# Optimization experiments

Hardware: AMD Instinct MI355X
Metric: run time of the kernel (lower is better)

## Reference

```python
import jax, jax.numpy as jnp
import numpy as np

L, B, N, C, H = 6, 4, 512, 512, 8
D = C // H          # head_dim = 64
MLP = 4 * C         # mlp_ratio = 4.0
EPS = 1e-6


def setup_inputs() -> dict:
    key = jax.random.key(0)
    ks = jax.random.split(key, 12)
    p = lambda k, sh: jax.random.normal(k, sh, dtype=jnp.float32) * 0.02
    return {
        "x": jax.random.normal(ks[0], (B, N, C), dtype=jnp.float32),
        "time_emb": jax.random.normal(ks[1], (B, C), dtype=jnp.float32),
        "pair_emb": jax.random.normal(ks[2], (B, H, N, N), dtype=jnp.float32) * 0.1,
        "is_padded_mask": jnp.zeros((B, 1, 1, N), dtype=bool),
        # per-block stacked params (leading dim = L blocks)
        "wq": p(ks[3], (L, C, C)),
        "wk": p(ks[4], (L, C, C)),
        "wv": p(ks[5], (L, C, C)),
        "wo": p(ks[6], (L, C, C)),
        "bo": jnp.zeros((L, C), dtype=jnp.float32),
        "w1": p(ks[7], (L, C, MLP)),
        "b1": jnp.zeros((L, MLP), dtype=jnp.float32),
        "w2": p(ks[8], (L, MLP, C)),
        "b2": jnp.zeros((L, C), dtype=jnp.float32),
        "wada": p(ks[9], (L, C, 6 * C)),
        "bada": jnp.zeros((L, 6 * C), dtype=jnp.float32),
    }


def _ln(x):
    # LayerNorm without affine, eps=1e-6 (torch elementwise_affine=False)
    mu = jnp.mean(x, axis=-1, keepdims=True)
    var = jnp.mean(jnp.square(x - mu), axis=-1, keepdims=True)
    return (x - mu) * jax.lax.rsqrt(var + EPS)


def _modulate(x, shift, scale):
    return x * (1.0 + scale[:, None, :]) + shift[:, None, :]


def reference(x, time_emb, pair_emb, is_padded_mask,
              wq, wk, wv, wo, bo, w1, b1, w2, b2, wada, bada):
    scale = D ** -0.5
    t_act = jax.nn.silu(time_emb)  # shared SiLU input to adaLN of each block
    for i in range(L):
        ada = t_act @ wada[i] + bada[i]  # (B, 6C)
        sh_msa, sc_msa, g_msa, sh_mlp, sc_mlp, g_mlp = jnp.split(ada, 6, axis=1)
        # fill_attn_mask: masked_fill padded key positions with -inf
        pair = jnp.where(is_padded_mask, -jnp.inf, pair_emb)  # (B,H,N,N)
        mx = _modulate(_ln(x), sh_msa, sc_msa)  # (B,N,C)
        q = (mx @ wq[i]).reshape(B, N, H, D)
        k = (mx @ wk[i]).reshape(B, N, H, D)
        v = (mx @ wv[i]).reshape(B, N, H, D)
        qk = jnp.einsum('bnhd,bshd->bhns', q, k) * scale  # (B,H,N,N)
        attn = jax.nn.softmax(qk + pair, axis=-1)
        o = jnp.einsum('bhns,bshd->bnhd', attn, v).reshape(B, N, C)
        o = o @ wo[i] + bo[i]
        x = x + g_msa[:, None, :] * o
        pair_emb = pair + qk  # residual on pair embedding
        h = _modulate(_ln(x), sh_mlp, sc_mlp)
        h = jax.nn.gelu(h @ w1[i] + b1[i], approximate=True) @ w2[i] + b2[i]
        x = x + g_mlp[:, None, :] * h
    return x, pair_emb
```

## Files before the change

### kernel.cpp

```cpp
#include <hip/hip_runtime.h>
#include <hip/hip_bf16.h>

#define LNUM 6
#define BB 4
#define NSEQ 512
#define CDIM 512
#define HNUM 8
#define DHEAD 64
#define MLPD 2048
#define MROWS (BB*NSEQ)

typedef __hip_bfloat16 bf16;
typedef __attribute__((ext_vector_type(4))) float f32x4;
typedef __attribute__((ext_vector_type(8))) short bf16x8;

__device__ __forceinline__ void gld_lds16(const bf16* g, bf16* l) {
  __builtin_amdgcn_global_load_lds((const __attribute__((address_space(1))) void*)g,
                                   (__attribute__((address_space(3))) void*)l, 16, 0, 0);
}

__device__ __forceinline__ float gelu_tanh(float t) {
  float u = 0.7978845608028654f * (t + 0.044715f * t * t * t);
  u = fminf(fmaxf(u, -15.f), 15.f);
  float e = __expf(2.f * u);
  return 0.5f * t * (1.f + (e - 1.f) / (e + 1.f));
}

enum { EP_BF16 = 0, EP_RESID = 2, EP_GELU = 3, EP_QKV = 4 };

template<int BM, int BN, int MODE>
__global__ __launch_bounds__(256) void gemm_nt(
    const bf16* __restrict__ A, int lda,
    const bf16* __restrict__ Bt, int ldb,
    int K, int zdiv,
    long sA1, long sA2, long sB1, long sB2, long sO1, long sO2,
    bf16* __restrict__ obf, int ldo,
    const float* __restrict__ bias,
    const float* __restrict__ ada, int gate_off,
    float* __restrict__ xres,
    bf16* __restrict__ vtout)
{
  constexpr int FM = BM / 32, FN = BN / 32;
  __shared__ bf16 lA[2 * BM * 64];
  __shared__ bf16 lB[2 * BN * 64];
  const int tid = threadIdx.x;
  const int wid = tid >> 6, lane = tid & 63;
  const int z = blockIdx.z;
  const long z1 = z / zdiv, z2 = z % zdiv;
  A  += z1 * sA1 + z2 * sA2;
  Bt += z1 * sB1 + z2 * sB2;
  const long obase = z1 * sO1 + z2 * sO2;
  const int m0 = blockIdx.x * BM;
  const int n0 = blockIdx.y * BN;
  const int wm = wid >> 1, wn = wid & 1;
  const int srow = tid >> 3, scl = tid & 7;

  f32x4 zero = {0.f, 0.f, 0.f, 0.f};
  f32x4 acc[FM][FN];
#pragma unroll
  for (int i = 0; i < FM; i++)
#pragma unroll
    for (int j = 0; j < FN; j++) acc[i][j] = zero;

  auto stage = [&](int buf, int kt) {
#pragma unroll
    for (int p = 0; p < BM / 32; p++) {
      const int rr = (p << 5) + srow;
      const int gk = (scl ^ (rr & 7)) << 3;
      gld_lds16(A + (size_t)(m0 + rr) * lda + (kt << 6) + gk,
                lA + buf * (BM * 64) + (p << 11) + (wid << 9));
    }
#pragma unroll
    for (int p = 0; p < BN / 32; p++) {
      const int rr = (p << 5) + srow;
      const int gk = (scl ^ (rr & 7)) << 3;
      gld_lds16(Bt + (size_t)(n0 + rr) * ldb + (kt << 6) + gk,
                lB + buf * (BN * 64) + (p << 11) + (wid << 9));
    }
  };

  const int rlo = lane & 15, kq = lane >> 4;
  auto compute = [&](int buf) {
#pragma unroll
    for (int kk = 0; kk < 2; kk++) {
      bf16x8 af[FM], bg[FN];
#pragma unroll
      for (int i = 0; i < FM; i++) {
        const int ra = wm * (BM / 2) + (i << 4) + rlo;
        af[i] = *(const bf16x8*)(lA + buf * (BM * 64) + (ra << 6) +
                                 ((((kk << 2) + kq) ^ (ra & 7)) << 3));
      }
#pragma unroll
      for (int j = 0; j < FN; j++) {
        const int rb2 = wn * (BN / 2) + (j << 4) + rlo;
        bg[j] = *(const bf16x8*)(lB + buf * (BN * 64) + (rb2 << 6) +
                                 ((((kk << 2) + kq) ^ (rb2 & 7)) << 3));
      }
#pragma unroll
      for (int i = 0; i < FM; i++)
#pragma unroll
        for (int j = 0; j < FN; j++)
          acc[i][j] = __builtin_amdgcn_mfma_f32_16x16x32_bf16(af[i], bg[j], acc[i][j], 0, 0, 0);
    }
  };

  const int NT = K >> 6;
  stage(0, 0);
  for (int t = 0; t < NT - 1; t++) {
    stage((t + 1) & 1, t + 1);
    constexpr int NL = (BM + BN) / 32;
    if constexpr (NL == 3)      asm volatile("s_waitcnt vmcnt(3)" ::: "memory");
    else if constexpr (NL == 4) asm volatile("s_waitcnt vmcnt(4)" ::: "memory");
    else if constexpr (NL == 6) asm volatile("s_waitcnt vmcnt(6)" ::: "memory");
    else                        asm volatile("s_waitcnt vmcnt(8)" ::: "memory");
    __builtin_amdgcn_s_barrier();
    asm volatile("" ::: "memory");
    compute(t & 1);
    asm volatile("" ::: "memory");
    __builtin_amdgcn_s_barrier();
  }
  asm volatile("s_waitcnt vmcnt(0)" ::: "memory");
  __builtin_amdgcn_s_barrier();
  asm volatile("" ::: "memory");
  compute((NT - 1) & 1);

  const int cl = lane & 15, rb = (lane >> 4) << 2;

  if (MODE == EP_QKV && n0 >= 2 * CDIM) {
    asm volatile("" ::: "memory");
    __builtin_amdgcn_s_barrier();
    bf16* lT = lA;
#pragma unroll
    for (int i = 0; i < FM; i++)
#pragma unroll
      for (int j = 0; j < FN; j++)
#pragma unroll
        for (int r = 0; r < 4; r++) {
          const int ln = wm * (BM / 2) + (i << 4) + rb + r;
          const int ld = wn * (BN / 2) + (j << 4) + cl;
          lT[ld * 72 + ln] = __float2bfloat16(acc[i][j][r]);
        }
    asm volatile("" ::: "memory");
    __builtin_amdgcn_s_barrier();
    const int b = m0 >> 9, nn = m0 & 511, h = (n0 - 2 * CDIM) >> 6;
    bf16* dst = vtout + ((size_t)(b * 8 + h) * 64) * 512;
    const int d = tid >> 2, nc = (tid & 3) << 4;
    bf16x8 v0 = *(const bf16x8*)(lT + d * 72 + nc);
    bf16x8 v1 = *(const bf16x8*)(lT + d * 72 + nc + 8);
    *(bf16x8*)(dst + (size_t)d * 512 + nn + nc) = v0;
    *(bf16x8*)(dst + (size_t)d * 512 + nn + nc + 8) = v1;
    return;
  }

#pragma unroll
  for (int i = 0; i < FM; i++) {
#pragma unroll
    for (int j = 0; j < FN; j++) {
      const int gc = n0 + wn * (BN / 2) + (j << 4) + cl;
#pragma unroll
      for (int r = 0; r < 4; r++) {
        const int gr = m0 + wm * (BM / 2) + (i << 4) + rb + r;
        float v = acc[i][j][r];
        if (MODE == EP_BF16 || MODE == EP_QKV) {
          obf[obase + (size_t)gr * ldo + gc] = __float2bfloat16(v);
        } else if (MODE == EP_RESID) {
          const int b = gr >> 9;
          float t2 = v + bias[gc];
          xres[(size_t)gr * CDIM + gc] += ada[b * (6 * CDIM) + gate_off + gc] * t2;
        } else {
          float t2 = v + bias[gc];
          obf[obase + (size_t)gr * ldo + gc] = __float2bfloat16(gelu_tanh(t2));
        }
      }
    }
  }
}

__global__ __launch_bounds__(256) void attn_fused(
    const bf16* __restrict__ qkv, const bf16* __restrict__ vt,
    const float* __restrict__ pair_in, float* __restrict__ pair_out,
    const unsigned char* __restrict__ mask,
    bf16* __restrict__ obuf, float scale)
{
  __shared__ bf16 lQ[64 * 64];
  __shared__ bf16 lK[2][64 * 64];
  __shared__ bf16 lV[2][64 * 64];
  __shared__ bf16 lP[64 * 64];
  const int tid = threadIdx.x, wid = tid >> 6, lane = tid & 63;
  const int z = blockIdx.z, b = z >> 3, h = z & 7;
  const int m0 = blockIdx.x * 64;
  const int srow = tid >> 3, scl = tid & 7;
  const bf16* Aq = qkv + (size_t)b * NSEQ * 1536 + h * 64;
  const bf16* Bk = Aq + CDIM;
  const bf16* Bv = vt + (size_t)z * DHEAD * NSEQ;
  const size_t pz = (size_t)z * NSEQ * NSEQ;
  const int rlo = lane & 15, kq = lane >> 4, cl = rlo;

#pragma unroll
  for (int r = 0; r < 2; r++) {
    const int rr = (r << 5) + srow;
    const int gk = (scl ^ (rr & 7)) << 3;
    gld_lds16(Aq + (size_t)(m0 + rr) * 1536 + gk, lQ + (r << 11) + (wid << 9));
    gld_lds16(Bk + (size_t)rr * 1536 + gk, lK[0] + (r << 11) + (wid << 9));
    gld_lds16(Bv + (size_t)rr * NSEQ + gk, lV[0] + (r << 11) + (wid << 9));
  }

  float m_run[4], l_run[4];
  f32x4 oacc[4];
  f32x4 zero = {0.f, 0.f, 0.f, 0.f};
#pragma unroll
  for (int r = 0; r < 4; r++) { m_run[r] = -INFINITY; l_run[r] = 0.f; }
#pragma unroll
  for (int j = 0; j < 4; j++) oacc[j] = zero;
  bf16x8 afq[2];

  for (int ct = 0; ct < 8; ct++) {
    const int cur = ct & 1;
    asm volatile("s_waitcnt vmcnt(0)" ::: "memory");
    __builtin_amdgcn_s_barrier();
    asm volatile("" ::: "memory");

    if (ct == 0) {
#pragma unroll
      for (int kk = 0; kk < 2; kk++) {
        const int ra = (wid << 4) + rlo;
        afq[kk] = *(const bf16x8*)(lQ + (ra << 6) + ((((kk << 2) + kq) ^ (ra & 7)) << 3));
      }
    }

    if (ct < 7) {
#pragma unroll
      for (int r = 0; r < 2; r++) {
        const int rr = (r << 5) + srow;
        const int gk = (scl ^ (rr & 7)) << 3;
        gld_lds16(Bk + (size_t)((ct + 1) * 64 + rr) * 1536 + gk,
                  lK[cur ^ 1] + (r << 11) + (wid << 9));
        gld_lds16(Bv + (size_t)rr * NSEQ + (ct + 1) * 64 + gk,
                  lV[cur ^ 1] + (r << 11) + (wid << 9));
      }
    }

    float pr[4][4];
#pragma unroll
    for (int j = 0; j < 4; j++)
#pragma unroll
      for (int r = 0; r < 4; r++)
        pr[j][r] = pair_in[pz + (size_t)(m0 + (wid << 4) + (kq << 2) + r) * NSEQ +
                           (ct * 64 + (j << 4) + cl)];
    bool mk[4];
#pragma unroll
    for (int j = 0; j < 4; j++)
      mk[j] = mask[b * NSEQ + ct * 64 + (j << 4) + cl] != 0;

    f32x4 s[4];
#pragma unroll
    for (int j = 0; j < 4; j++) s[j] = zero;
#pragma unroll
    for (int kk = 0; kk < 2; kk++)
#pragma unroll
      for (int j = 0; j < 4; j++) {
        const int rk = (j << 4) + rlo;
        bf16x8 bk = *(const bf16x8*)(lK[cur] + (rk << 6) + ((((kk << 2) + kq) ^ (rk & 7)) << 3));
        s[j] = __builtin_amdgcn_mfma_f32_16x16x32_bf16(afq[kk], bk, s[j], 0, 0, 0);
      }

    float p[4][4];
#pragma unroll
    for (int r = 0; r < 4; r++) {
      const size_t prow = pz + (size_t)(m0 + (wid << 4) + (kq << 2) + r) * NSEQ + ct * 64;
      float sf[4];
#pragma unroll
      for (int j = 0; j < 4; j++) {
        float pp = mk[j] ? -INFINITY : pr[j][r];
        sf[j] = s[j][r] * scale + pp;
        pair_out[prow + (j << 4) + cl] = sf[j];
      }
      float tm = fmaxf(fmaxf(sf[0], sf[1]), fmaxf(sf[2], sf[3]));
#pragma unroll
      for (int o = 1; o < 16; o <<= 1) tm = fmaxf(tm, __shfl_xor(tm, o));
      const float mnew = fmaxf(m_run[r], tm);
      const float fr = __expf(m_run[r] - mnew);
      float rs = 0.f;
#pragma unroll
      for (int j = 0; j < 4; j++) { p[j][r] = __expf(sf[j] - mnew); rs += p[j][r]; }
#pragma unroll
      for (int o = 1; o < 16; o <<= 1) rs += __shfl_xor(rs, o);
      l_run[r] = l_run[r] * fr + rs;
      m_run[r] = mnew;
#pragma unroll
      for (int j = 0; j < 4; j++) oacc[j][r] *= fr;
    }

#pragma unroll
    for (int j = 0; j < 4; j++)
#pragma unroll
      for (int r = 0; r < 4; r++) {
        const int row = (wid << 4) + (kq << 2) + r;
        const int col = (j << 4) + cl;
        lP[(row << 6) + (((col >> 3) ^ (row & 7)) << 3) + (col & 7)] = __float2bfloat16(p[j][r]);
      }
    asm volatile("s_waitcnt lgkmcnt(0)" ::: "memory");
    __builtin_amdgcn_sched_barrier(0);

#pragma unroll
    for (int kk = 0; kk < 2; kk++) {
      const int ra = (wid << 4) + rlo;
      bf16x8 ap = *(const bf16x8*)(lP + (ra << 6) + ((((kk << 2) + kq) ^ (ra & 7)) << 3));
#pragma unroll
      for (int j = 0; j < 4; j++) {
        const int rd = (j << 4) + rlo;
        bf16x8 bv = *(const bf16x8*)(lV[cur] + (rd << 6) + ((((kk << 2) + kq) ^ (rd & 7)) << 3));
        oacc[j] = __builtin_amdgcn_mfma_f32_16x16x32_bf16(ap, bv, oacc[j], 0, 0, 0);
      }
    }
  }

#pragma unroll
  for (int j = 0; j < 4; j++)
#pragma unroll
    for (int r = 0; r < 4; r++) {
      const int gr = m0 + (wid << 4) + (kq << 2) + r;
      const int gc = h * 64 + (j << 4) + cl;
      obuf[((size_t)b * NSEQ + gr) * CDIM + gc] = __float2bfloat16(oacc[j][r] / l_run[r]);
    }
}

__global__ __launch_bounds__(256) void ln_mod(const float* __restrict__ x,
                                              const float* __restrict__ ada,
                                              int sh_off, int sc_off,
                                              bf16* __restrict__ out)
{
  const int row = blockIdx.x;
  const int b = row >> 9;
  const float* xr = x + (size_t)row * CDIM;
  const int t = threadIdx.x;
  float2 v = ((const float2*)xr)[t];
  float s = v.x + v.y;
  float ss = v.x * v.x + v.y * v.y;
#pragma unroll
  for (int o = 32; o > 0; o >>= 1) { s += __shfl_down(s, o); ss += __shfl_down(ss, o); }
  __shared__ float red[8];
  __shared__ float mv[2];
  const int w = t >> 6, ln = t & 63;
  if (ln == 0) { red[w] = s; red[4 + w] = ss; }
  __syncthreads();
  if (t == 0) {
    float S = red[0] + red[1] + red[2] + red[3];
    float SS = red[4] + red[5] + red[6] + red[7];
    float mu = S * (1.0f / CDIM);
    float var = SS * (1.0f / CDIM) - mu * mu;
    mv[0] = mu; mv[1] = rsqrtf(var + 1e-6f);
  }
  __syncthreads();
  const float mu = mv[0], rs = mv[1];
  const float* adab = ada + b * (6 * CDIM);
  const int c = t * 2;
  float o0 = (v.x - mu) * rs * (1.0f + adab[sc_off + c])     + adab[sh_off + c];
  float o1 = (v.y - mu) * rs * (1.0f + adab[sc_off + c + 1]) + adab[sh_off + c + 1];
  out[(size_t)row * CDIM + c]     = __float2bfloat16(o0);
  out[(size_t)row * CDIM + c + 1] = __float2bfloat16(o1);
}

__global__ __launch_bounds__(256) void ada_part(const float* __restrict__ te,
                                                const float* __restrict__ wada,
                                                float* __restrict__ partial)
{
  __shared__ float ta[4][64];
  const int layer = blockIdx.z, kc = blockIdx.y;
  const int t = threadIdx.x;
  {
    const int b = t >> 6, kk = t & 63;
    float xx = te[b * CDIM + kc * 64 + kk];
    ta[b][kk] = xx / (1.f + __expf(-xx));
  }
  __syncthreads();
  const int col = blockIdx.x * 512 + t * 2;
  const float* W = wada + ((size_t)layer * CDIM + kc * 64) * 3072 + col;
  float2 acc0 = {0, 0}, acc1 = {0, 0}, acc2 = {0, 0}, acc3 = {0, 0};
#pragma unroll 8
  for (int kk = 0; kk < 64; kk++) {
    float2 w = *(const float2*)(W + (size_t)kk * 3072);
    acc0.x = fmaf(ta[0][kk], w.x, acc0.x); acc0.y = fmaf(ta[0][kk], w.y, acc0.y);
    acc1.x = fmaf(ta[1][kk], w.x, acc1.x); acc1.y = fmaf(ta[1][kk], w.y, acc1.y);
    acc2.x = fmaf(ta[2][kk], w.x, acc2.x); acc2.y = fmaf(ta[2][kk], w.y, acc2.y);
    acc3.x = fmaf(ta[3][kk], w.x, acc3.x); acc3.y = fmaf(ta[3][kk], w.y, acc3.y);
  }
  float* pp = partial + (((size_t)(layer * 8 + kc) * 4) * 3072);
  *(float2*)(pp + 0 * 3072 + col) = acc0;
  *(float2*)(pp + 1 * 3072 + col) = acc1;
  *(float2*)(pp + 2 * 3072 + col) = acc2;
  *(float2*)(pp + 3 * 3072 + col) = acc3;
}

__global__ __launch_bounds__(256) void ada_reduce(const float* __restrict__ partial,
                                                  const float* __restrict__ bada,
                                                  float* __restrict__ adab)
{
  const int idx = blockIdx.x * 256 + threadIdx.x;
  const int layer = idx / 12288, rem = idx % 12288;
  const int b = rem / 3072, col = rem % 3072;
  float acc = bada[layer * 3072 + col];
#pragma unroll
  for (int kc = 0; kc < 8; kc++)
    acc += partial[((size_t)(layer * 8 + kc) * 4 + b) * 3072 + col];
  adab[((size_t)layer * 4 + b) * 3072 + col] = acc;
}

__global__ __launch_bounds__(256) void conv_t(const float* __restrict__ src, bf16* __restrict__ dst,
                                              int R, int Ccols, long sS, long sD)
{
  src += (size_t)blockIdx.z * sS;
  dst += (size_t)blockIdx.z * sD;
  __shared__ float tb[32][33];
  const int c0 = blockIdx.x * 32, r0 = blockIdx.y * 32;
  const int tx = threadIdx.x & 31, ty = threadIdx.x >> 5;
#pragma unroll
  for (int i = ty; i < 32; i += 8) tb[i][tx] = src[(size_t)(r0 + i) * Ccols + c0 + tx];
  __syncthreads();
#pragma unroll
  for (int i = ty; i < 32; i += 8) dst[(size_t)(c0 + i) * R + r0 + tx] = __float2bfloat16(tb[tx][i]);
}

extern "C" void kernel_launch(void* const* d_in, const int* in_sizes, int n_in,
                              void* d_out, int out_size, void* d_ws, size_t ws_size,
                              hipStream_t stream)
{
  (void)in_sizes; (void)n_in; (void)out_size; (void)ws_size;
  const float* in_x    = (const float*)d_in[0];
  const float* in_te   = (const float*)d_in[1];
  const float* in_pair = (const float*)d_in[2];
  const unsigned char* in_mask = (const unsigned char*)d_in[3];
  const float* wq   = (const float*)d_in[4];
  const float* wk   = (const float*)d_in[5];
  const float* wv   = (const float*)d_in[6];
  const float* wo   = (const float*)d_in[7];
  const float* bo   = (const float*)d_in[8];
  const float* w1   = (const float*)d_in[9];
  const float* b1   = (const float*)d_in[10];
  const float* w2   = (const float*)d_in[11];
  const float* b2   = (const float*)d_in[12];
  const float* wada = (const float*)d_in[13];
  const float* bada = (const float*)d_in[14];

  float* xout = (float*)d_out;
  float* pairout = xout + (size_t)BB * NSEQ * CDIM;

  char* ws = (char*)d_ws;
  size_t off = 0;
  auto alloc = [&](size_t bytes) -> void* {
    void* p = ws + off; off += (bytes + 255) & ~(size_t)255; return p;
  };
  bf16*  wqkvT = (bf16*)alloc((size_t)LNUM * 1536 * 512 * 2);
  bf16*  woT   = (bf16*)alloc((size_t)LNUM * 512 * 512 * 2);
  bf16*  w1T   = (bf16*)alloc((size_t)LNUM * 2048 * 512 * 2);
  bf16*  w2T   = (bf16*)alloc((size_t)LNUM * 512 * 2048 * 2);
  float* adab  = (float*)alloc((size_t)LNUM * BB * 6 * CDIM * 4);
  float* apart = (float*)alloc((size_t)LNUM * 8 * BB * 3072 * 4);
  bf16*  mx    = (bf16*)alloc((size_t)MROWS * CDIM * 2);
  bf16*  qkv   = (bf16*)alloc((size_t)MROWS * 1536 * 2);
  bf16*  vt    = (bf16*)alloc((size_t)BB * HNUM * DHEAD * NSEQ * 2);
  bf16*  obuf  = (bf16*)alloc((size_t)MROWS * CDIM * 2);
  bf16*  hbuf  = (bf16*)alloc((size_t)MROWS * MLPD * 2);

  hipMemcpyAsync(xout, in_x, (size_t)MROWS * CDIM * 4, hipMemcpyDeviceToDevice, stream);

  conv_t<<<dim3(16, 16, LNUM), 256, 0, stream>>>(wq, wqkvT,               512, 512,  (long)512 * 512,  (long)1536 * 512);
  conv_t<<<dim3(16, 16, LNUM), 256, 0, stream>>>(wk, wqkvT + 512 * 512,   512, 512,  (long)512 * 512,  (long)1536 * 512);
  conv_t<<<dim3(16, 16, LNUM), 256, 0, stream>>>(wv, wqkvT + 2 * 512 * 512, 512, 512, (long)512 * 512, (long)1536 * 512);
  conv_t<<<dim3(16, 16, LNUM), 256, 0, stream>>>(wo, woT,                 512, 512,  (long)512 * 512,  (long)512 * 512);
  conv_t<<<dim3(64, 16, LNUM), 256, 0, stream>>>(w1, w1T,                 512, 2048, (long)512 * 2048, (long)2048 * 512);
  conv_t<<<dim3(16, 64, LNUM), 256, 0, stream>>>(w2, w2T,                 2048, 512, (long)2048 * 512, (long)512 * 2048);

  ada_part<<<dim3(6, 8, LNUM), 256, 0, stream>>>(in_te, wada, apart);
  ada_reduce<<<dim3(LNUM * BB * 3072 / 256), 256, 0, stream>>>(apart, bada, adab);

  const float scale = 0.125f;
  for (int i = 0; i < LNUM; i++) {
    const float* adal = adab + (size_t)i * BB * 6 * CDIM;
    ln_mod<<<MROWS, 256, 0, stream>>>(xout, adal, 0, CDIM, mx);
    gemm_nt<64, 64, EP_QKV><<<dim3(32, 24, 1), 256, 0, stream>>>(
        mx, CDIM, wqkvT + (size_t)i * 1536 * 512, CDIM, CDIM, 1,
        0, 0, 0, 0, 0, 0,
        qkv, 1536, nullptr, nullptr, 0, nullptr, vt);
    const float* pin = (i == 0) ? in_pair : pairout;
    attn_fused<<<dim3(8, 1, 32), 256, 0, stream>>>(qkv, vt, pin, pairout, in_mask, obuf, scale);
    gemm_nt<32, 64, EP_RESID><<<dim3(64, 8, 1), 256, 0, stream>>>(
        obuf, CDIM, woT + (size_t)i * CDIM * CDIM, CDIM, CDIM, 1,
        0, 0, 0, 0, 0, 0,
        nullptr, CDIM, bo + (size_t)i * CDIM, adal, 2 * CDIM, xout, nullptr);
    ln_mod<<<MROWS, 256, 0, stream>>>(xout, adal, 3 * CDIM, 4 * CDIM, mx);
    gemm_nt<64, 64, EP_GELU><<<dim3(32, 32, 1), 256, 0, stream>>>(
        mx, CDIM, w1T + (size_t)i * MLPD * CDIM, CDIM, CDIM, 1,
        0, 0, 0, 0, 0, 0,
        hbuf, MLPD, b1 + (size_t)i * MLPD, nullptr, 0, nullptr, nullptr);
    gemm_nt<32, 64, EP_RESID><<<dim3(64, 8, 1), 256, 0, stream>>>(
        hbuf, MLPD, w2T + (size_t)i * CDIM * MLPD, MLPD, MLPD, 1,
        0, 0, 0, 0, 0, 0,
        nullptr, CDIM, b2 + (size_t)i * CDIM, adal, 5 * CDIM, xout, nullptr);
  }
}
```

Baseline: 523.7 us.

## Triple-buffer GEMM K-loop, drop x copy, merge QKV/O weight transposes

The GEMM main loop moves from double to triple buffering in LDS. Loads now run two K-tiles ahead, with wait counts graded by how many tiles remain, and the trailing barrier on the last iteration is dropped. The device-to-device copy of x into the output is removed: the first layer reads in_x directly, and the residual epilogue writes xsrc+gate*t instead of read-modify-write on xout. The four 512x512 weight transposes are merged into one launch. The costs are more LDS per block, which may lower occupancy, and some added control logic.

```diff
diff --git a/kernel.cpp b/kernel.cpp
--- a/kernel.cpp
+++ b/kernel.cpp
@@ -37,12 +37,13 @@
     bf16* __restrict__ obf, int ldo,
     const float* __restrict__ bias,
     const float* __restrict__ ada, int gate_off,
-    float* __restrict__ xres,
+    float* __restrict__ xres, const float* __restrict__ xsrc,
     bf16* __restrict__ vtout)
 {
   constexpr int FM = BM / 32, FN = BN / 32;
-  __shared__ bf16 lA[2 * BM * 64];
-  __shared__ bf16 lB[2 * BN * 64];
+  constexpr int NL = (BM + BN) / 32;
+  __shared__ bf16 lA[3 * BM * 64];
+  __shared__ bf16 lB[3 * BN * 64];
   const int tid = threadIdx.x;
   const int wid = tid >> 6, lane = tid & 63;
   const int z = blockIdx.z;
@@ -106,23 +107,25 @@
 
   const int NT = K >> 6;
   stage(0, 0);
-  for (int t = 0; t < NT - 1; t++) {
-    stage((t + 1) & 1, t + 1);
-    constexpr int NL = (BM + BN) / 32;
-    if constexpr (NL == 3)      asm volatile("s_waitcnt vmcnt(3)" ::: "memory");
-    else if constexpr (NL == 4) asm volatile("s_waitcnt vmcnt(4)" ::: "memory");
-    else if constexpr (NL == 6) asm volatile("s_waitcnt vmcnt(6)" ::: "memory");
-    else                        asm volatile("s_waitcnt vmcnt(8)" ::: "memory");
+  if (NT > 1) stage(1, 1);
+  for (int t = 0; t < NT; t++) {
+    if (t + 2 < NT) stage((t + 2) % 3, t + 2);
+    const int ahead = NT - 1 - t;
+    if (ahead >= 2) {
+      if constexpr (NL == 3) asm volatile("s_waitcnt vmcnt(6)" ::: "memory");
+      else                   asm volatile("s_waitcnt vmcnt(8)" ::: "memory");
+    } else if (ahead == 1) {
+      if constexpr (NL == 3) asm volatile("s_waitcnt vmcnt(3)" ::: "memory");
+      else                   asm volatile("s_waitcnt vmcnt(4)" ::: "memory");
+    } else {
+      asm volatile("s_waitcnt vmcnt(0)" ::: "memory");
+    }
     __builtin_amdgcn_s_barrier();
     asm volatile("" ::: "memory");
-    compute(t & 1);
+    compute(t % 3);
     asm volatile("" ::: "memory");
-    __builtin_amdgcn_s_barrier();
-  }
-  asm volatile("s_waitcnt vmcnt(0)" ::: "memory");
-  __builtin_amdgcn_s_barrier();
-  asm volatile("" ::: "memory");
-  compute((NT - 1) & 1);
+    if (t + 1 < NT) __builtin_amdgcn_s_barrier();
+  }
 
   const int cl = lane & 15, rb = (lane >> 4) << 2;
 
@@ -166,7 +169,8 @@
         } else if (MODE == EP_RESID) {
           const int b = gr >> 9;
           float t2 = v + bias[gc];
-          xres[(size_t)gr * CDIM + gc] += ada[b * (6 * CDIM) + gate_off + gc] * t2;
+          xres[(size_t)gr * CDIM + gc] =
+              xsrc[(size_t)gr * CDIM + gc] + ada[b * (6 * CDIM) + gate_off + gc] * t2;
         } else {
           float t2 = v + bias[gc];
           obf[obase + (size_t)gr * ldo + gc] = __float2bfloat16(gelu_tanh(t2));
@@ -404,6 +408,29 @@
   for (int kc = 0; kc < 8; kc++)
     acc += partial[((size_t)(layer * 8 + kc) * 4 + b) * 3072 + col];
   adab[((size_t)layer * 4 + b) * 3072 + col] = acc;
+}
+
+__global__ __launch_bounds__(256) void conv_t4(const float* __restrict__ s0,
+                                               const float* __restrict__ s1,
+                                               const float* __restrict__ s2,
+                                               const float* __restrict__ s3,
+                                               bf16* __restrict__ dqkv,
+                                               bf16* __restrict__ dwo)
+{
+  const int zi = blockIdx.z;
+  const int mat = zi / LNUM, layer = zi % LNUM;
+  const float* src = (mat == 0 ? s0 : mat == 1 ? s1 : mat == 2 ? s2 : s3) +
+                     (size_t)layer * 512 * 512;
+  bf16* dst = (mat < 3) ? (dqkv + (size_t)layer * 1536 * 512 + (size_t)mat * 512 * 512)
+                        : (dwo + (size_t)layer * 512 * 512);
+  __shared__ float tb[32][33];
+  const int c0 = blockIdx.x * 32, r0 = blockIdx.y * 32;
+  const int tx = threadIdx.x & 31, ty = threadIdx.x >> 5;
+#pragma unroll
+  for (int i = ty; i < 32; i += 8) tb[i][tx] = src[(size_t)(r0 + i) * 512 + c0 + tx];
+  __syncthreads();
+#pragma unroll
+  for (int i = ty; i < 32; i += 8) dst[(size_t)(c0 + i) * 512 + r0 + tx] = __float2bfloat16(tb[tx][i]);
 }
 
 __global__ __launch_bounds__(256) void conv_t(const float* __restrict__ src, bf16* __restrict__ dst,
@@ -462,14 +489,9 @@
   bf16*  obuf  = (bf16*)alloc((size_t)MROWS * CDIM * 2);
   bf16*  hbuf  = (bf16*)alloc((size_t)MROWS * MLPD * 2);
 
-  hipMemcpyAsync(xout, in_x, (size_t)MROWS * CDIM * 4, hipMemcpyDeviceToDevice, stream);
-
-  conv_t<<<dim3(16, 16, LNUM), 256, 0, stream>>>(wq, wqkvT,               512, 512,  (long)512 * 512,  (long)1536 * 512);
-  conv_t<<<dim3(16, 16, LNUM), 256, 0, stream>>>(wk, wqkvT + 512 * 512,   512, 512,  (long)512 * 512,  (long)1536 * 512);
-  conv_t<<<dim3(16, 16, LNUM), 256, 0, stream>>>(wv, wqkvT + 2 * 512 * 512, 512, 512, (long)512 * 512, (long)1536 * 512);
-  conv_t<<<dim3(16, 16, LNUM), 256, 0, stream>>>(wo, woT,                 512, 512,  (long)512 * 512,  (long)512 * 512);
-  conv_t<<<dim3(64, 16, LNUM), 256, 0, stream>>>(w1, w1T,                 512, 2048, (long)512 * 2048, (long)2048 * 512);
-  conv_t<<<dim3(16, 64, LNUM), 256, 0, stream>>>(w2, w2T,                 2048, 512, (long)2048 * 512, (long)512 * 2048);
+  conv_t4<<<dim3(16, 16, 4 * LNUM), 256, 0, stream>>>(wq, wk, wv, wo, wqkvT, woT);
+  conv_t<<<dim3(64, 16, LNUM), 256, 0, stream>>>(w1, w1T, 512, 2048, (long)512 * 2048, (long)2048 * 512);
+  conv_t<<<dim3(16, 64, LNUM), 256, 0, stream>>>(w2, w2T, 2048, 512, (long)2048 * 512, (long)512 * 2048);
 
   ada_part<<<dim3(6, 8, LNUM), 256, 0, stream>>>(in_te, wada, apart);
   ada_reduce<<<dim3(LNUM * BB * 3072 / 256), 256, 0, stream>>>(apart, bada, adab);
@@ -477,25 +499,26 @@
   const float scale = 0.125f;
   for (int i = 0; i < LNUM; i++) {
     const float* adal = adab + (size_t)i * BB * 6 * CDIM;
-    ln_mod<<<MROWS, 256, 0, stream>>>(xout, adal, 0, CDIM, mx);
+    const float* xin = (i == 0) ? in_x : xout;
+    ln_mod<<<MROWS, 256, 0, stream>>>(xin, adal, 0, CDIM, mx);
     gemm_nt<64, 64, EP_QKV><<<dim3(32, 24, 1), 256, 0, stream>>>(
         mx, CDIM, wqkvT + (size_t)i * 1536 * 512, CDIM, CDIM, 1,
         0, 0, 0, 0, 0, 0,
-        qkv, 1536, nullptr, nullptr, 0, nullptr, vt);
+        qkv, 1536, nullptr, nullptr, 0, nullptr, nullptr, vt);
     const float* pin = (i == 0) ? in_pair : pairout;
     attn_fused<<<dim3(8, 1, 32), 256, 0, stream>>>(qkv, vt, pin, pairout, in_mask, obuf, scale);
     gemm_nt<32, 64, EP_RESID><<<dim3(64, 8, 1), 256, 0, stream>>>(
         obuf, CDIM, woT + (size_t)i * CDIM * CDIM, CDIM, CDIM, 1,
         0, 0, 0, 0, 0, 0,
-        nullptr, CDIM, bo + (size_t)i * CDIM, adal, 2 * CDIM, xout, nullptr);
+        nullptr, CDIM, bo + (size_t)i * CDIM, adal, 2 * CDIM, xout, xin, nullptr);
     ln_mod<<<MROWS, 256, 0, stream>>>(xout, adal, 3 * CDIM, 4 * CDIM, mx);
     gemm_nt<64, 64, EP_GELU><<<dim3(32, 32, 1), 256, 0, stream>>>(
         mx, CDIM, w1T + (size_t)i * MLPD * CDIM, CDIM, CDIM, 1,
         0, 0, 0, 0, 0, 0,
-        hbuf, MLPD, b1 + (size_t)i * MLPD, nullptr, 0, nullptr, nullptr);
+        hbuf, MLPD, b1 + (size_t)i * MLPD, nullptr, 0, nullptr, nullptr, nullptr);
     gemm_nt<32, 64, EP_RESID><<<dim3(64, 8, 1), 256, 0, stream>>>(
         hbuf, MLPD, w2T + (size_t)i * CDIM * MLPD, MLPD, MLPD, 1,
         0, 0, 0, 0, 0, 0,
-        nullptr, CDIM, b2 + (size_t)i * CDIM, adal, 5 * CDIM, xout, nullptr);
-  }
-}
+        nullptr, CDIM, b2 + (size_t)i * CDIM, adal, 5 * CDIM, xout, xout, nullptr);
+  }
+}
```

New measurement: 552.4 us. 1.05x slower.
